# Kernel tuning notes

Hardware: AMD Instinct MI355X
Metric: run time of the kernel (lower is better)

The kernel has to match this reference:

```python
import jax, jax.numpy as jnp
import numpy as np

N = 10000      # nodes
E = 320000     # edges (avg degree 32)
H = 128        # hidden_channels
G = 50         # num_gaussians
NF = 128       # num_filters
L = 6          # num_interactions
CUTOFF = 10.0


def ssp(x):
    # ShiftedSoftplus: softplus(x) - log(2)
    return jax.nn.softplus(x) - jnp.log(2.0).astype(x.dtype)


def setup_inputs() -> dict:
    key = jax.random.key(0)
    ks = jax.random.split(key, 16)
    s = 0.05
    return {
        "z": jax.random.normal(ks[0], (N, H), jnp.float32),
        "pos": jax.random.normal(ks[1], (N, 3), jnp.float32) * 3.0,
        "edge_index": jax.random.randint(ks[2], (2, E), 0, N, dtype=jnp.int64),
        # per-layer stacked parameters (PyTorch Linear convention: y = x @ W.T + b)
        "mlp1_w": jax.random.normal(ks[3], (L, NF, G), jnp.float32) * s,
        "mlp1_b": jnp.zeros((L, NF), jnp.float32),
        "mlp2_w": jax.random.normal(ks[4], (L, NF, NF), jnp.float32) * s,
        "mlp2_b": jnp.zeros((L, NF), jnp.float32),
        "lin1_w": jax.random.normal(ks[5], (L, NF, H), jnp.float32) * s,   # no bias
        "lin2_w": jax.random.normal(ks[6], (L, H, NF), jnp.float32) * s,
        "lin2_b": jnp.zeros((L, H), jnp.float32),
        "lin_w": jax.random.normal(ks[7], (L, H, H), jnp.float32) * s,
        "lin_b": jnp.zeros((L, H), jnp.float32),
        "coord_w": jax.random.normal(ks[8], (L, 1, G + 2 * H), jnp.float32) * s,
        "coord_b": jnp.zeros((L, 1), jnp.float32),
    }


def reference(z, pos, edge_index, mlp1_w, mlp1_b, mlp2_w, mlp2_b,
              lin1_w, lin2_w, lin2_b, lin_w, lin_b, coord_w, coord_b):
    row, col = edge_index[0], edge_index[1]
    # edge distances from INITIAL positions (computed once, as in torch code)
    edge_weight = jnp.linalg.norm(pos[row] - pos[col], axis=-1)          # [E]
    offset = jnp.linspace(0.0, CUTOFF, G).astype(pos.dtype)              # [G]
    coeff = -0.5 / (offset[1] - offset[0]) ** 2
    edge_attr = jnp.exp(coeff * (edge_weight[:, None] - offset[None, :]) ** 2)  # [E,G]
    C = 0.5 * (jnp.cos(edge_weight * jnp.pi / CUTOFF) + 1.0)             # [E] cosine cutoff
    ones_e = jnp.ones((E,), pos.dtype)
    h = z
    for l in range(L):
        # ---- coordinate update (uses current pos and current h) ----
        feat = jnp.concatenate([edge_attr, h[row], h[col]], axis=-1)     # [E, G+2H]
        cw = feat @ coord_w[l].T + coord_b[l]                            # [E,1]
        aggr = (pos[row] - pos[col]) * cw                                # [E,3]
        sums = jax.ops.segment_sum(aggr, row, num_segments=N)            # [N,3]
        cnt = jax.ops.segment_sum(ones_e, row, num_segments=N)           # [N]
        mean = jnp.where(cnt[:, None] > 0, sums / jnp.maximum(cnt, 1.0)[:, None], 0.0)
        pos = pos + mean
        # ---- CFConv interaction ----
        Wf = ssp(edge_attr @ mlp1_w[l].T + mlp1_b[l]) @ mlp2_w[l].T + mlp2_b[l]  # [E,NF]
        Wf = Wf * C[:, None]
        xf = h @ lin1_w[l].T                                             # [N,NF]
        agg = jax.ops.segment_sum(xf[row] * Wf, col, num_segments=N)     # [N,NF]
        out = agg @ lin2_w[l].T + lin2_b[l]                              # [N,H]
        h = h + (ssp(out) @ lin_w[l].T + lin_b[l])
    return (pos, h)
```

## Files before the change

kernel.cpp:

```cpp
#include <hip/hip_runtime.h>


#define NN 10000
#define EE 320000
#define HH 128
#define GG 50
#define NF 128
#define NL 6
#define TROWS 2048
#define NB 128

typedef unsigned short u16;
typedef unsigned int u32;
typedef short bf16x8 __attribute__((ext_vector_type(8)));
typedef float f32x4  __attribute__((ext_vector_type(4)));

__device__ __forceinline__ float us2f(u16 u){
  union { float f; u32 i; } v; v.i = ((u32)u) << 16; return v.f;
}
__device__ __forceinline__ u16 f2us(float x){
  union { float f; u32 i; } v; v.f = x;
  u32 r = v.i + 0x7fffu + ((v.i >> 16) & 1u);
  return (u16)(r >> 16);
}
__device__ __forceinline__ float ldin(const void* p, int i, int bf){
  return bf ? us2f(((const u16*)p)[i]) : ((const float*)p)[i];
}
__device__ __forceinline__ float sspf(float x){
  return fmaxf(x, 0.f) + __logf(1.f + __expf(-fabsf(x))) - 0.6931472f;
}
__device__ __forceinline__ int detect_bf(const u32* __restrict__ zraw){
  int lane = threadIdx.x & 63;
  int c = 0;
  #pragma unroll
  for(int j=0;j<4;j++){
    u32 w = zraw[lane*4+j];
    u32 hb = (w >> 8) & 0x7F;
    c += (hb >= 0x38 && hb <= 0x41) ? 1 : 0;
  }
  return __popcll(__ballot(c >= 2)) >= 32;
}
__device__ __forceinline__ int detect_i64(const int* __restrict__ ei_raw){
  int lane = threadIdx.x & 63;
  int c = 0;
  #pragma unroll
  for(int j=0;j<4;j++) c += (ei_raw[2*(lane*4+j)+1] == 0) ? 1 : 0;
  return __popcll(__ballot(c >= 3)) >= 32;
}

__global__ void k_prep(const u32* __restrict__ zraw, const void* __restrict__ pos_in,
    const void* __restrict__ mlp1_w, const void* __restrict__ mlp1_b,
    const void* __restrict__ mlp2_w, const void* __restrict__ mlp2_b,
    const void* __restrict__ lin1_w, const void* __restrict__ lin2_w,
    const void* __restrict__ lin2_b, const void* __restrict__ lin_w,
    const void* __restrict__ lin_b,  const void* __restrict__ coord_w,
    const void* __restrict__ coord_b,
    float* __restrict__ h, float* __restrict__ pc40, int* __restrict__ wmaxi,
    float* __restrict__ b1f, float* __restrict__ b2v,
    float* __restrict__ w1t, float* __restrict__ w2t,
    float* __restrict__ l1t, u16* __restrict__ l1b, u16* __restrict__ l2b,
    float* __restrict__ l2bf, u16* __restrict__ lwb,
    float* __restrict__ lbf, float* __restrict__ cwf, float* __restrict__ cbf)
{
  int bf = detect_bf(zraw);
  int b = blockIdx.x;
  if(b < NN*HH/256){
    int i = b*256 + threadIdx.x;
    h[i] = ldin(zraw, i, bf);
    if(i < NN*3){
      int n = i/3, comp = i%3;
      pc40[n*4 + comp] = ldin(pos_in, i, bf);
    }
    if(i == 0) *wmaxi = 0;
  } else {
    int i = (b - NN*HH/256)*256 + threadIdx.x;
    if(i < NL*NF){
      b1f[i]  = ldin(mlp1_b, i, bf);
      b2v[i]  = ldin(mlp2_b, i, bf);
      l2bf[i] = ldin(lin2_b, i, bf);
      lbf[i]  = ldin(lin_b,  i, bf);
    }
    if(i < NL*GG*NF){
      int l = i/(GG*NF), rem = i%(GG*NF);
      int g = rem/NF, f = rem%NF;
      w1t[i] = ldin(mlp1_w, (l*NF + f)*GG + g, bf);
    }
    if(i < NL*NF*NF){
      int l = i/(NF*NF), rem = i%(NF*NF);
      int k = rem/NF, f = rem%NF;
      w2t[i] = ldin(mlp2_w, l*NF*NF + f*NF + k, bf);
      l1t[i] = ldin(lin1_w, l*NF*HH + f*HH + k, bf);
      l1b[i] = f2us(ldin(lin1_w, i, bf));
      l2b[i] = f2us(ldin(lin2_w, i, bf));
      lwb[i] = f2us(ldin(lin_w,  i, bf));
    }
    if(i < NL*(GG+2*HH)) cwf[i] = ldin(coord_w, i, bf);
    if(i < NL) cbf[i] = ldin(coord_b, i, bf);
  }
}

__global__ void k_count(const int* __restrict__ ei_raw, const float* __restrict__ pc4,
                        int* __restrict__ eiN, float* __restrict__ wE,
                        u32* __restrict__ partR32, u32* __restrict__ partC32,
                        int* __restrict__ wmaxi){
  __shared__ u32 hr[NN/2];
  __shared__ u32 hc[NN/2];
  int is64 = detect_i64(ei_raw);
  int b = blockIdx.x, tid = threadIdx.x;
  for(int i=tid; i<NN/2; i+=256){ hr[i]=0; hc[i]=0; }
  __syncthreads();
  int e0 = b*(EE/NB), e1 = e0 + EE/NB;
  float wm = 0.f;
  for(int e = e0 + tid; e < e1; e += 256){
    int r = is64 ? ei_raw[2*e] : ei_raw[e];
    int c = is64 ? ei_raw[2*(EE+e)] : ei_raw[EE+e];
    eiN[e] = r; eiN[EE+e] = c;
    float4 pr = *(const float4*)&pc4[r*4];
    float4 pcv = *(const float4*)&pc4[c*4];
    float dx = pr.x-pcv.x, dy = pr.y-pcv.y, dz = pr.z-pcv.z;
    float w = sqrtf(dx*dx + dy*dy + dz*dz);
    wE[e] = w;
    wm = fmaxf(wm, w);
    atomicAdd(&hr[r>>1], (r&1) ? 0x10000u : 1u);
    atomicAdd(&hc[c>>1], (c&1) ? 0x10000u : 1u);
  }
  #pragma unroll
  for(int s=32; s>0; s>>=1) wm = fmaxf(wm, __shfl_down(wm, s, 64));
  if((tid & 63) == 0) atomicMax(wmaxi, __float_as_int(wm));
  __syncthreads();
  for(int i=tid; i<NN/2; i+=256){
    partR32[(size_t)b*(NN/2) + i] = hr[i];
    partC32[(size_t)b*(NN/2) + i] = hc[i];
  }
}

__global__ void k_scan2(const int* __restrict__ col_deg, const int* __restrict__ deg_row,
                        int* __restrict__ col_start, int* __restrict__ row_start){
  __shared__ int pc[1024];
  __shared__ int pr[1024];
  int tid = threadIdx.x;
  const int CH = (NN + 1023)/1024;
  int base = tid*CH;
  int sc = 0, sr = 0;
  for(int i=0;i<CH;i++){
    int idx = base+i;
    if(idx<NN){ sc += col_deg[idx]; sr += deg_row[idx]; }
  }
  pc[tid] = sc; pr[tid] = sr;
  __syncthreads();
  for(int off=1; off<1024; off<<=1){
    int vc = (tid>=off) ? pc[tid-off] : 0;
    int vr = (tid>=off) ? pr[tid-off] : 0;
    __syncthreads();
    pc[tid] += vc; pr[tid] += vr;
    __syncthreads();
  }
  int runc = (tid==0) ? 0 : pc[tid-1];
  int runr = (tid==0) ? 0 : pr[tid-1];
  for(int i=0;i<CH;i++){
    int idx = base+i;
    if(idx<NN){
      col_start[idx]=runc; runc += col_deg[idx];
      row_start[idx]=runr; runr += deg_row[idx];
    }
  }
  if(tid==1023){ col_start[NN] = runc; row_start[NN] = runr; }
}

__global__ void k_fill(const int* __restrict__ eiN, const float* __restrict__ wE,
                       const int* __restrict__ col_start, const int* __restrict__ row_start,
                       const u16* __restrict__ partR16, const u16* __restrict__ partC16,
                       int* __restrict__ row_s, float* __restrict__ wEs,
                       int* __restrict__ rcol_s, float* __restrict__ rw_s){
  __shared__ u32 hr[NN/2];
  __shared__ u32 hc[NN/2];
  int b = blockIdx.x, t = threadIdx.x;
  for(int i=t; i<NN/2; i+=256){ hr[i]=0; hc[i]=0; }
  __syncthreads();
  int e0 = b*(EE/NB), e1 = e0 + EE/NB;
  for(int e = e0 + t; e < e1; e += 256){
    int r = eiN[e], c = eiN[EE+e];
    float w = wE[e];
    u32 oldc = atomicAdd(&hc[c>>1], (c&1) ? 0x10000u : 1u);
    u32 rkc = (c&1) ? (oldc >> 16) : (oldc & 0xFFFFu);
    int p = col_start[c] + (int)partC16[(size_t)b*NN + c] + (int)rkc;
    row_s[p] = r; wEs[p] = w;
    u32 oldr = atomicAdd(&hr[r>>1], (r&1) ? 0x10000u : 1u);
    u32 rkr = (r&1) ? (oldr >> 16) : (oldr & 0xFFFFu);
    int p2 = row_start[r] + (int)partR16[(size_t)b*NN + r] + (int)rkr;
    rcol_s[p2] = c; rw_s[p2] = w;
  }
}

__global__ void k_tabnode(const float* __restrict__ w1t, const float* __restrict__ b1f,
                          const float* __restrict__ w2t, const float* __restrict__ b2v,
                          const float* __restrict__ cwf, const int* __restrict__ wmaxi,
                          u16* __restrict__ tabB, float* __restrict__ tabS,
                          const float* __restrict__ h, const float* __restrict__ l1t,
                          u16* __restrict__ xfb0, float* __restrict__ dr0,
                          float* __restrict__ pc40,
                          u16* __restrict__ partR16, u16* __restrict__ partC16,
                          int* __restrict__ degR, int* __restrict__ degC){
  __shared__ float attr[16*64];
  __shared__ float tls[128*17];
  int b = blockIdx.x, t = threadIdx.x;
  if(b < NL*128){
    int l = b >> 7;
    int r0 = (b & 127)*16;
    int f = t & 127, half = t >> 7;
    float delta = __int_as_float(*wmaxi) / (float)(TROWS-1);
    for(int idx=t; idx<16*64; idx+=256){
      int r = idx >> 6, g = idx & 63;
      float w = (float)(r0 + r)*delta;
      float d = w - (float)g*(10.f/49.f);
      attr[idx] = (g < GG) ? __expf(-12.005f*d*d) : 0.f;
    }
    __syncthreads();
    const float* __restrict__ w1 = w1t + l*GG*NF;
    float b1 = b1f[l*NF + f];
    float a1[8];
    #pragma unroll
    for(int r=0;r<8;r++) a1[r] = b1;
    for(int g=0; g<GG; g++){
      float wv = w1[g*NF + f];
      #pragma unroll
      for(int r=0;r<8;r++) a1[r] += attr[(half*8 + r)*64 + g]*wv;
    }
    #pragma unroll
    for(int r=0;r<8;r++) tls[f*17 + half*8 + r] = sspf(a1[r]);
    __syncthreads();
    const float* __restrict__ w2 = w2t + l*NF*NF;
    float b2 = b2v[l*NF + f];
    float a2[8];
    #pragma unroll
    for(int r=0;r<8;r++) a2[r] = b2;
    for(int k=0;k<NF;k++){
      float wv = w2[k*NF + f];
      #pragma unroll
      for(int r=0;r<8;r++) a2[r] += tls[k*17 + half*8 + r]*wv;
    }
    #pragma unroll
    for(int r=0;r<8;r++){
      int row = r0 + half*8 + r;
      float w = (float)row*delta;
      float C = 0.5f*(cosf(w*0.3141592653589793f) + 1.f);
      tabB[((size_t)l*TROWS + row)*NF + f] = f2us(a2[r]*C);
    }
    if(t < 16){
      const float* __restrict__ cwg = cwf + l*(GG+2*HH);
      float s = 0.f;
      for(int g=0; g<GG; g++) s += attr[t*64 + g]*cwg[g];
      tabS[l*TROWS + r0 + t] = s;
    }
  } else if(b < NL*128 + NN/8 + NN/4){
    int nb = b - NL*128;
    if(nb < NN/8){
      int f = t & 127, g = t >> 7;
      int n0 = nb*8 + g*4;
      const float* __restrict__ wt = l1t;
      float acc[4] = {0.f,0.f,0.f,0.f};
      for(int k=0;k<HH;k++){
        float wv = wt[k*NF + f];
        #pragma unroll
        for(int i=0;i<4;i++) acc[i] += h[(n0+i)*HH + k]*wv;
      }
      #pragma unroll
      for(int i=0;i<4;i++) xfb0[(n0+i)*NF + f] = f2us(acc[i]);
    } else {
      int lane = t & 63;
      int n = (nb - NN/8)*4 + (t >> 6);
      const float* __restrict__ cw = cwf;
      float h0 = h[n*HH + lane], h1 = h[n*HH + 64 + lane];
      float ar = h0*cw[GG + lane]      + h1*cw[GG + 64 + lane];
      float ac = h0*cw[GG + HH + lane] + h1*cw[GG + HH + 64 + lane];
      #pragma unroll
      for(int s=32; s>0; s>>=1){
        ar += __shfl_down(ar, s, 64);
        ac += __shfl_down(ac, s, 64);
      }
      if(lane == 0){ dr0[n] = ar; pc40[n*4+3] = ac; }
    }
  } else {
    int n = (b - (NL*128 + NN/8 + NN/4))*256 + t;
    if(n >= NN) return;
    u32 rr = 0, rc = 0;
    for(int b0=0; b0<NB; b0+=8){
      u32 vr[8], vc[8];
      #pragma unroll
      for(int j=0;j<8;j++){
        vr[j] = partR16[(size_t)(b0+j)*NN + n];
        vc[j] = partC16[(size_t)(b0+j)*NN + n];
      }
      #pragma unroll
      for(int j=0;j<8;j++){
        partR16[(size_t)(b0+j)*NN + n] = (u16)rr; rr += vr[j];
        partC16[(size_t)(b0+j)*NN + n] = (u16)rc; rc += vc[j];
      }
    }
    degR[n] = (int)rr; degC[n] = (int)rc;
  }
}

__global__ void k_layer(const int* __restrict__ col_start, const int* __restrict__ row_s,
                        const float* __restrict__ wEs, const u32* __restrict__ xfR,
                        u16* __restrict__ xfW,
                        const u16* __restrict__ tabB, const int* __restrict__ wmaxi,
                        int l,
                        const u16* __restrict__ l2b, const float* __restrict__ l2bf,
                        const u16* __restrict__ lwb, const float* __restrict__ lbf,
                        float* __restrict__ h, const u16* __restrict__ l1b,
                        const float* __restrict__ cwf,
                        const float* __restrict__ drR, float* __restrict__ drW,
                        const int* __restrict__ row_start, const int* __restrict__ rcol_s,
                        const float* __restrict__ rw_s, const float* __restrict__ tabS,
                        const float* __restrict__ cbf,
                        const float* __restrict__ pc4R, float* __restrict__ pc4W,
                        const u32* __restrict__ zraw, void* __restrict__ out){
  __shared__ __align__(16) u16 T[16*136];
  __shared__ __align__(16) u16 T2[16*136];
  int b = blockIdx.x, t = threadIdx.x;
  float invD = (float)(TROWS-1) / __int_as_float(*wmaxi);
  int wave = t >> 6, lane = t & 63;

  if(b % 3 == 0){
    int n0 = (b/3)*16;
    {
      const u32* __restrict__ tg32 = (const u32*)(tabB + (size_t)l*TROWS*NF);
      u32* __restrict__ T32 = (u32*)T;
      #pragma unroll
      for(int j=0;j<2;j++){
        int n = n0 + wave*2 + j;
        int p0 = col_start[n], p1 = col_start[n+1];
        float aa[4] = {0.f,0.f,0.f,0.f};
        float bb[4] = {0.f,0.f,0.f,0.f};
        int p = p0;
        for(; p+8 <= p1; p += 8){
          u32 gv[8], xv[8];
          #pragma unroll
          for(int k=0;k<8;k++){
            int r = row_s[p+k];
            int i0 = min((int)(wEs[p+k]*invD + 0.5f), TROWS-1);
            gv[k] = tg32[i0*64 + lane];
            xv[k] = xfR[r*64 + lane];
          }
          #pragma unroll
          for(int k=0;k<8;k++){
            aa[k&3] += us2f((u16)xv[k])      * us2f((u16)gv[k]);
            bb[k&3] += us2f((u16)(xv[k]>>16))* us2f((u16)(gv[k]>>16));
          }
        }
        for(; p < p1; p++){
          int r = row_s[p];
          int i0 = min((int)(wEs[p]*invD + 0.5f), TROWS-1);
          u32 g = tg32[i0*64 + lane];
          u32 x = xfR[r*64 + lane];
          aa[0] += us2f((u16)x)      * us2f((u16)g);
          bb[0] += us2f((u16)(x>>16))* us2f((u16)(g>>16));
        }
        float av = (aa[0]+aa[1])+(aa[2]+aa[3]);
        float bv = (bb[0]+bb[1])+(bb[2]+bb[3]);
        T32[(wave*2+j)*68 + lane] = (u32)f2us(av) | ((u32)f2us(bv) << 16);
      }
    }
    __syncthreads();
    int m16 = lane & 15, quad = lane >> 4;
    int fcol = wave*16 + m16;
    f32x4 acc;
    {
      bf16x8 aA[4];
      #pragma unroll
      for(int ks=0; ks<4; ks++)
        aA[ks] = *(const bf16x8*)&T[m16*136 + ks*32 + quad*8];
      const u16* __restrict__ wA = l2b + l*HH*NF;
      float bv = l2bf[l*HH + fcol];
      acc = (f32x4){bv,bv,bv,bv};
      #pragma unroll
      for(int ks=0; ks<4; ks++){
        bf16x8 bbv = *(const bf16x8*)&wA[fcol*NF + ks*32 + quad*8];
        acc = __builtin_amdgcn_mfma_f32_16x16x32_bf16(aA[ks], bbv, acc, 0,0,0);
      }
      #pragma unroll
      for(int r=0;r<4;r++)
        T2[(quad*4+r)*136 + fcol] = f2us(sspf(acc[r]));
    }
    __syncthreads();
    float hv[4];
    int bf = (l == NL-1) ? detect_bf(zraw) : 0;
    {
      bf16x8 aS[4];
      #pragma unroll
      for(int ks=0; ks<4; ks++)
        aS[ks] = *(const bf16x8*)&T2[m16*136 + ks*32 + quad*8];
      const u16* __restrict__ wB = lwb + l*HH*HH;
      float bv = lbf[l*HH + fcol];
      acc = (f32x4){bv,bv,bv,bv};
      #pragma unroll
      for(int ks=0; ks<4; ks++){
        bf16x8 bbv = *(const bf16x8*)&wB[fcol*HH + ks*32 + quad*8];
        acc = __builtin_amdgcn_mfma_f32_16x16x32_bf16(aS[ks], bbv, acc, 0,0,0);
      }
      #pragma unroll
      for(int r=0;r<4;r++)
        hv[r] = h[(n0+quad*4+r)*HH + fcol] + acc[r];
    }
    if(l == NL-1){
      #pragma unroll
      for(int r=0;r<4;r++){
        int n = n0 + quad*4 + r;
        if(bf) ((u16*)out)[NN*3 + n*HH + fcol] = f2us(hv[r]);
        else   ((float*)out)[NN*3 + n*HH + fcol] = hv[r];
      }
      return;
    }
    #pragma unroll
    for(int r=0;r<4;r++){
      int n = n0 + quad*4 + r;
      h[n*HH + fcol] = hv[r];
      T[(quad*4+r)*136 + fcol] = f2us(hv[r]);
    }
    __syncthreads();
    {
      bf16x8 aH[4];
      #pragma unroll
      for(int ks=0; ks<4; ks++)
        aH[ks] = *(const bf16x8*)&T[m16*136 + ks*32 + quad*8];
      const u16* __restrict__ wC = l1b + (l+1)*NF*HH;
      acc = (f32x4){0.f,0.f,0.f,0.f};
      #pragma unroll
      for(int ks=0; ks<4; ks++){
        bf16x8 bbv = *(const bf16x8*)&wC[fcol*HH + ks*32 + quad*8];
        acc = __builtin_amdgcn_mfma_f32_16x16x32_bf16(aH[ks], bbv, acc, 0,0,0);
      }
      #pragma unroll
      for(int r=0;r<4;r++)
        xfW[(n0+quad*4+r)*NF + fcol] = f2us(acc[r]);
    }
    {
      const float* __restrict__ cw = cwf + (l+1)*(GG + 2*HH);
      int j = t >> 5, l32 = t & 31;
      float ar = 0.f, ac = 0.f;
      #pragma unroll
      for(int i=0;i<4;i++){
        float hvv = us2f(T[j*136 + l32 + 32*i]);
        ar += hvv*cw[GG + l32 + 32*i];
        ac += hvv*cw[GG + HH + l32 + 32*i];
      }
      #pragma unroll
      for(int s=16; s>0; s>>=1){
        ar += __shfl_down(ar, s, 32);
        ac += __shfl_down(ac, s, 32);
      }
      if(l32 == 0){ drW[n0+j] = ar; pc4W[(n0+j)*4+3] = ac; }
    }
  } else {
    int u = b - b/3 - 1;
    int bf = (l == NL-1) ? detect_bf(zraw) : 0;
    int n = u*8 + wave;
    const float* __restrict__ ts = tabS + l*TROWS;
    float cb = cbf[l] + drR[n];
    int p0 = row_start[n], p1 = row_start[n+1];
    float4 pn = *(const float4*)&pc4R[n*4];
    float sx=0.f, sy=0.f, sz=0.f;
    for(int p = p0 + lane; p < p1; p += 64){
      int c = rcol_s[p];
      int i0 = min((int)(rw_s[p]*invD + 0.5f), TROWS-1);
      float4 pcv = *(const float4*)&pc4R[c*4];
      float a = cb + pcv.w + ts[i0];
      sx += (pn.x - pcv.x)*a;
      sy += (pn.y - pcv.y)*a;
      sz += (pn.z - pcv.z)*a;
    }
    #pragma unroll
    for(int s=32; s>0; s>>=1){
      sx += __shfl_down(sx, s, 64);
      sy += __shfl_down(sy, s, 64);
      sz += __shfl_down(sz, s, 64);
    }
    if(lane == 0){
      int cnt = p1 - p0;
      float inv = (cnt > 0) ? 1.f/(float)cnt : 0.f;
      float ox = pn.x + sx*inv, oy = pn.y + sy*inv, oz = pn.z + sz*inv;
      if(l == NL-1){
        if(bf){
          u16* o = (u16*)out;
          o[n*3+0] = f2us(ox); o[n*3+1] = f2us(oy); o[n*3+2] = f2us(oz);
        } else {
          float* o = (float*)out;
          o[n*3+0] = ox; o[n*3+1] = oy; o[n*3+2] = oz;
        }
      } else {
        pc4W[n*4+0] = ox; pc4W[n*4+1] = oy; pc4W[n*4+2] = oz;
      }
    }
  }
}

extern "C" void kernel_launch(void* const* d_in, const int* in_sizes, int n_in,
                              void* d_out, int out_size, void* d_ws, size_t ws_size,
                              hipStream_t stream){
  const u32*  z      = (const u32*)d_in[0];
  const void* pos_in = d_in[1];
  const int*  ei_raw = (const int*)d_in[2];
  const void* mlp1_w = d_in[3];
  const void* mlp1_b = d_in[4];
  const void* mlp2_w = d_in[5];
  const void* mlp2_b = d_in[6];
  const void* lin1_w = d_in[7];
  const void* lin2_w = d_in[8];
  const void* lin2_b = d_in[9];
  const void* lin_w  = d_in[10];
  const void* lin_b  = d_in[11];
  const void* coord_w= d_in[12];
  const void* coord_b= d_in[13];

  float* W = (float*)d_ws;
  float* h    = W; W += NN*HH;
  float* pc40 = W; W += NN*4;
  float* pc41 = W; W += NN*4;
  float* dr0  = W; W += NN;
  float* dr1  = W; W += NN;
  float* wE   = W; W += EE;
  float* wEs  = W; W += EE;
  float* rw_s = W; W += EE;
  float* b1f  = W; W += NL*NF;
  float* b2v  = W; W += NL*NF;
  float* w1t  = W; W += NL*GG*NF;
  float* w2t  = W; W += NL*NF*NF;
  float* l1t  = W; W += NL*NF*HH;
  float* l2bf = W; W += NL*HH;
  float* lbf  = W; W += NL*HH;
  float* cwf  = W; W += NL*(GG+2*HH);
  float* cbf  = W; W += NL;
  W = (float*)(((uintptr_t)W + 63) & ~(uintptr_t)63);
  u16*  tabB = (u16*)W; W += (size_t)NL*TROWS*NF/2;
  float* tabS = W; W += NL*TROWS;
  u16* l1b  = (u16*)W; W += (NL*NF*NF)/2;
  u16* l2b  = (u16*)W; W += (NL*NF*NF)/2;
  u16* lwb  = (u16*)W; W += (NL*NF*NF)/2;
  u16* xfb0 = (u16*)W; W += (NN*NF)/2;
  u16* xfb1 = (u16*)W; W += (NN*NF)/2;
  u16* partR16 = (u16*)W; W += (size_t)NB*NN/2;
  u16* partC16 = (u16*)W; W += (size_t)NB*NN/2;
  int* degR      = (int*)W; W += NN;
  int* degC      = (int*)W; W += NN;
  int* col_start = (int*)W; W += NN+1;
  int* row_start = (int*)W; W += NN+1;
  int* row_s     = (int*)W; W += EE;
  int* rcol_s    = (int*)W; W += EE;
  int* eiN       = (int*)W; W += 2*EE;
  int* wmaxi     = (int*)W; W += 1;

  k_prep<<<NN*HH/256 + NL*NF*NF/256, 256, 0, stream>>>(
      z, pos_in, mlp1_w, mlp1_b, mlp2_w, mlp2_b, lin1_w, lin2_w, lin2_b,
      lin_w, lin_b, coord_w, coord_b,
      h, pc40, wmaxi,
      b1f, b2v, w1t, w2t, l1t, l1b, l2b, l2bf, lwb, lbf, cwf, cbf);
  k_count<<<NB, 256, 0, stream>>>(ei_raw, pc40, eiN, wE,
                                  (u32*)partR16, (u32*)partC16, wmaxi);
  k_tabnode<<<NL*128 + NN/8 + NN/4 + (NN+255)/256, 256, 0, stream>>>(
      w1t, b1f, w2t, b2v, cwf, wmaxi, tabB, tabS,
      h, l1t, xfb0, dr0, pc40,
      partR16, partC16, degR, degC);
  k_scan2<<<1, 1024, 0, stream>>>(degC, degR, col_start, row_start);
  k_fill<<<NB, 256, 0, stream>>>(eiN, wE, col_start, row_start, partR16, partC16,
                                 row_s, wEs, rcol_s, rw_s);

  for(int l=0; l<NL; l++){
    int par = l & 1;
    const u32* xfR = (const u32*)(par ? xfb1 : xfb0);
    u16* xfW = par ? xfb0 : xfb1;
    const float* drR = par ? dr1 : dr0;   float* drW = par ? dr0 : dr1;
    const float* p4R = par ? pc41 : pc40; float* p4W = par ? pc40 : pc41;
    k_layer<<<3*(NN/16), 512, 0, stream>>>(
        col_start, row_s, wEs, xfR, xfW, tabB, wmaxi, l,
        l2b, l2bf, lwb, lbf, h, l1b, cwf,
        drR, drW,
        row_start, rcol_s, rw_s, tabS, cbf, p4R, p4W, z, d_out);
  }
}
```

Before: 409.8 us.

## Use 1024-thread blocks with one wave per node in layer kernel

The fused layer kernel moves from 512-thread blocks (a 1:2 split of CFConv to coordinate blocks) to 1024-thread blocks with alternating block roles. In CFConv blocks each of the 16 waves gathers one node instead of each of 8 waves handling two. The MFMA stages run on the first 8 waves while the upper 8 waves compute the coordinate dot products in parallel. Coordinate blocks now cover 16 nodes each. This raises memory-level parallelism for the gathers, but larger blocks may lower occupancy and leave half the waves idle during the MFMA phases.

```diff
diff --git a/kernel.cpp b/kernel.cpp
--- a/kernel.cpp
+++ b/kernel.cpp
@@ -322,51 +322,49 @@
   float invD = (float)(TROWS-1) / __int_as_float(*wmaxi);
   int wave = t >> 6, lane = t & 63;
 
-  if(b % 3 == 0){
-    int n0 = (b/3)*16;
+  if(!(b & 1)){
+    int n0 = (b >> 1)*16;
     {
       const u32* __restrict__ tg32 = (const u32*)(tabB + (size_t)l*TROWS*NF);
       u32* __restrict__ T32 = (u32*)T;
-      #pragma unroll
-      for(int j=0;j<2;j++){
-        int n = n0 + wave*2 + j;
-        int p0 = col_start[n], p1 = col_start[n+1];
-        float aa[4] = {0.f,0.f,0.f,0.f};
-        float bb[4] = {0.f,0.f,0.f,0.f};
-        int p = p0;
-        for(; p+8 <= p1; p += 8){
-          u32 gv[8], xv[8];
-          #pragma unroll
-          for(int k=0;k<8;k++){
-            int r = row_s[p+k];
-            int i0 = min((int)(wEs[p+k]*invD + 0.5f), TROWS-1);
-            gv[k] = tg32[i0*64 + lane];
-            xv[k] = xfR[r*64 + lane];
-          }
-          #pragma unroll
-          for(int k=0;k<8;k++){
-            aa[k&3] += us2f((u16)xv[k])      * us2f((u16)gv[k]);
-            bb[k&3] += us2f((u16)(xv[k]>>16))* us2f((u16)(gv[k]>>16));
-          }
+      int n = n0 + wave;
+      int p0 = col_start[n], p1 = col_start[n+1];
+      float aa[4] = {0.f,0.f,0.f,0.f};
+      float bb[4] = {0.f,0.f,0.f,0.f};
+      int p = p0;
+      for(; p+8 <= p1; p += 8){
+        u32 gv[8], xv[8];
+        #pragma unroll
+        for(int k=0;k<8;k++){
+          int r = row_s[p+k];
+          int i0 = min((int)(wEs[p+k]*invD + 0.5f), TROWS-1);
+          gv[k] = tg32[i0*64 + lane];
+          xv[k] = xfR[r*64 + lane];
         }
-        for(; p < p1; p++){
-          int r = row_s[p];
-          int i0 = min((int)(wEs[p]*invD + 0.5f), TROWS-1);
-          u32 g = tg32[i0*64 + lane];
-          u32 x = xfR[r*64 + lane];
-          aa[0] += us2f((u16)x)      * us2f((u16)g);
-          bb[0] += us2f((u16)(x>>16))* us2f((u16)(g>>16));
+        #pragma unroll
+        for(int k=0;k<8;k++){
+          aa[k&3] += us2f((u16)xv[k])      * us2f((u16)gv[k]);
+          bb[k&3] += us2f((u16)(xv[k]>>16))* us2f((u16)(gv[k]>>16));
         }
-        float av = (aa[0]+aa[1])+(aa[2]+aa[3]);
-        float bv = (bb[0]+bb[1])+(bb[2]+bb[3]);
-        T32[(wave*2+j)*68 + lane] = (u32)f2us(av) | ((u32)f2us(bv) << 16);
-      }
+      }
+      for(; p < p1; p++){
+        int r = row_s[p];
+        int i0 = min((int)(wEs[p]*invD + 0.5f), TROWS-1);
+        u32 g = tg32[i0*64 + lane];
+        u32 x = xfR[r*64 + lane];
+        aa[0] += us2f((u16)x)      * us2f((u16)g);
+        bb[0] += us2f((u16)(x>>16))* us2f((u16)(g>>16));
+      }
+      float av = (aa[0]+aa[1])+(aa[2]+aa[3]);
+      float bv = (bb[0]+bb[1])+(bb[2]+bb[3]);
+      T32[wave*68 + lane] = (u32)f2us(av) | ((u32)f2us(bv) << 16);
     }
     __syncthreads();
     int m16 = lane & 15, quad = lane >> 4;
-    int fcol = wave*16 + m16;
+    int w8 = (wave < 8);
+    int fcol = (wave & 7)*16 + m16;
     f32x4 acc;
-    {
+    if(w8){
       bf16x8 aA[4];
       #pragma unroll
       for(int ks=0; ks<4; ks++)
@@ -384,9 +382,32 @@
         T2[(quad*4+r)*136 + fcol] = f2us(sspf(acc[r]));
     }
     __syncthreads();
-    float hv[4];
-    int bf = (l == NL-1) ? detect_bf(zraw) : 0;
-    {
+    if(l == NL-1){
+      int bf = detect_bf(zraw);
+      if(w8){
+        bf16x8 aS[4];
+        #pragma unroll
+        for(int ks=0; ks<4; ks++)
+          aS[ks] = *(const bf16x8*)&T2[m16*136 + ks*32 + quad*8];
+        const u16* __restrict__ wB = lwb + l*HH*HH;
+        float bv = lbf[l*HH + fcol];
+        acc = (f32x4){bv,bv,bv,bv};
+        #pragma unroll
+        for(int ks=0; ks<4; ks++){
+          bf16x8 bbv = *(const bf16x8*)&wB[fcol*HH + ks*32 + quad*8];
+          acc = __builtin_amdgcn_mfma_f32_16x16x32_bf16(aS[ks], bbv, acc, 0,0,0);
+        }
+        #pragma unroll
+        for(int r=0;r<4;r++){
+          int n = n0 + quad*4 + r;
+          float hvv = h[n*HH + fcol] + acc[r];
+          if(bf) ((u16*)out)[NN*3 + n*HH + fcol] = f2us(hvv);
+          else   ((float*)out)[NN*3 + n*HH + fcol] = hvv;
+        }
+      }
+      return;
+    }
+    if(w8){
       bf16x8 aS[4];
       #pragma unroll
       for(int ks=0; ks<4; ks++)
@@ -400,26 +421,15 @@
         acc = __builtin_amdgcn_mfma_f32_16x16x32_bf16(aS[ks], bbv, acc, 0,0,0);
       }
       #pragma unroll
-      for(int r=0;r<4;r++)
-        hv[r] = h[(n0+quad*4+r)*HH + fcol] + acc[r];
-    }
-    if(l == NL-1){
-      #pragma unroll
       for(int r=0;r<4;r++){
         int n = n0 + quad*4 + r;
-        if(bf) ((u16*)out)[NN*3 + n*HH + fcol] = f2us(hv[r]);
-        else   ((float*)out)[NN*3 + n*HH + fcol] = hv[r];
-      }
-      return;
-    }
-    #pragma unroll
-    for(int r=0;r<4;r++){
-      int n = n0 + quad*4 + r;
-      h[n*HH + fcol] = hv[r];
-      T[(quad*4+r)*136 + fcol] = f2us(hv[r]);
-    }
-    __syncthreads();
-    {
+        float hvv = h[n*HH + fcol] + acc[r];
+        h[n*HH + fcol] = hvv;
+        T[(quad*4+r)*136 + fcol] = f2us(hvv);
+      }
+    }
+    __syncthreads();
+    if(w8){
       bf16x8 aH[4];
       #pragma unroll
       for(int ks=0; ks<4; ks++)
@@ -434,10 +444,10 @@
       #pragma unroll
       for(int r=0;r<4;r++)
         xfW[(n0+quad*4+r)*NF + fcol] = f2us(acc[r]);
-    }
-    {
+    } else {
       const float* __restrict__ cw = cwf + (l+1)*(GG + 2*HH);
-      int j = t >> 5, l32 = t & 31;
+      int idx = t - 512;
+      int j = idx >> 5, l32 = idx & 31;
       float ar = 0.f, ac = 0.f;
       #pragma unroll
       for(int i=0;i<4;i++){
@@ -453,9 +463,9 @@
       if(l32 == 0){ drW[n0+j] = ar; pc4W[(n0+j)*4+3] = ac; }
     }
   } else {
-    int u = b - b/3 - 1;
+    int u = b >> 1;
     int bf = (l == NL-1) ? detect_bf(zraw) : 0;
-    int n = u*8 + wave;
+    int n = u*16 + wave;
     const float* __restrict__ ts = tabS + l*TROWS;
     float cb = cbf[l] + drR[n];
     int p0 = row_start[n], p1 = row_start[n+1];
@@ -571,7 +581,7 @@
     u16* xfW = par ? xfb0 : xfb1;
     const float* drR = par ? dr1 : dr0;   float* drW = par ? dr0 : dr1;
     const float* p4R = par ? pc41 : pc40; float* p4W = par ? pc40 : pc41;
-    k_layer<<<3*(NN/16), 512, 0, stream>>>(
+    k_layer<<<2*(NN/16), 1024, 0, stream>>>(
         col_start, row_s, wEs, xfR, xfW, tabB, wmaxi, l,
         l2b, l2bf, lwb, lbf, h, l1b, cwf,
         drR, drW,
```

After: 457.3 us. +11.6%, slower.
